# Kernel optimization log

Measured on AMD Instinct MI355X. Metric: run time of the kernel, lower is better.

The kernel has to match this reference:

```python
import jax, jax.numpy as jnp
import numpy as np

H = 512; VT = 10000; VN = 1000; ET = 256; EN = 256
A = 50; B = 8; L = 128; SOS = 0


def setup_inputs():
    key = jax.random.key(0)
    ks = jax.random.split(key, 12)
    g = lambda k, s: jax.random.normal(k, s, jnp.float32) * 0.02
    inp = {}
    inp["n_tensor"] = jax.random.randint(ks[0], (B, L), 0, VN)
    inp["t_tensor"] = jax.random.randint(ks[1], (B, L), 0, VT)
    inp["p_tensor"] = jax.random.randint(ks[2], (B, L), 0, L)
    # embedding tables; padding rows (padding_idx) zeroed as nn.Embedding init does
    inp["embN"] = g(ks[3], (VN, EN)).at[VN - 1].set(0.0)
    inp["embT"] = g(ks[4], (VT + A + 3, ET)).at[VT - 1].set(0.0)
    inp["W_hid"] = g(ks[5], (H, H)); inp["b_hid"] = jnp.zeros((H,), jnp.float32)
    inp["W_mem"] = g(ks[6], (H, H)); inp["b_mem"] = jnp.zeros((H,), jnp.float32)
    inp["v_w"] = g(ks[7], (H,)); inp["v_b"] = jnp.zeros((), jnp.float32)
    inp["W_ih"] = g(ks[8], (4 * H, EN + ET)); inp["W_hh"] = g(ks[9], (4 * H, H))
    inp["b_ih"] = jnp.zeros((4 * H,), jnp.float32); inp["b_hh"] = jnp.zeros((4 * H,), jnp.float32)
    inp["W_g"] = g(ks[10], (3 * H, VT + 3)); inp["b_g"] = jnp.zeros((VT + 3,), jnp.float32)
    inp["W_s"] = g(ks[11], (2 * H,)); inp["b_s"] = jnp.zeros((), jnp.float32)
    return inp


def _forward(embN, embT, W_hid, b_hid, W_mem, b_mem, v_w, v_b,
             W_ih, W_hh, b_ih, b_hh, W_g, b_g, W_s, b_s,
             n_tensor, t_tensor, p_tensor):
    full_mask = (n_tensor == VN - 1)                      # [B, L] eof mask
    sos = jnp.full((B, 1), SOS, n_tensor.dtype)
    n_in = jnp.concatenate([sos, n_tensor[:, :-1]], 1)    # teacher-forced inputs
    t_in = jnp.concatenate([sos, t_tensor[:, :-1]], 1)
    par = jnp.concatenate([jnp.zeros((B, 1), p_tensor.dtype), p_tensor[:, :-1]], 1)
    hs0 = jnp.zeros((B, L, H), jnp.float32)               # growing memory buffer
    h0 = jnp.zeros((B, H), jnp.float32)
    c0 = jnp.zeros((B, H), jnp.float32)
    barange = jnp.arange(B)
    arangeA = jnp.arange(A)

    def step(carry, xs):
        hs, h, c = carry
        t, n_t, t_t, p_t, tgt = xs
        # embedding gathers + single-layer LSTM cell (torch gate order i,f,g,o)
        x = jnp.concatenate([embN[n_t], embT[t_t]], 1)    # [B, EN+ET]
        gates = x @ W_ih.T + h @ W_hh.T + (b_ih + b_hh)
        i, f, gg, o = jnp.split(gates, 4, axis=1)
        c = jax.nn.sigmoid(f) * c + jax.nn.sigmoid(i) * jnp.tanh(gg)
        h = jax.nn.sigmoid(o) * jnp.tanh(c)
        # sliding-window memory hs[:, max(t-A,0):t], fixed-size slice + validity mask
        s = jnp.maximum(t - A, 0)
        mem = jax.lax.dynamic_slice(hs, (0, s, 0), (B, A, H))   # [B, A, H]
        fm = jax.lax.dynamic_slice(full_mask, (0, s), (B, A))   # [B, A]
        valid = (s + arangeA) < t                               # [A] positions already written
        mask = fm | ~valid[None, :]
        # additive attention: v^T tanh(W_hid h + W_mem mem)
        sc = jnp.tanh((h @ W_hid.T + b_hid)[:, None, :] + mem @ W_mem.T + b_mem)
        sc = sc @ v_w + v_b                                     # [B, A]
        sc = jnp.where(mask, -1e20, sc)
        attn = jax.nn.softmax(sc, axis=1)
        context = jnp.einsum('ba,bah->bh', attn, mem)
        h_parent = hs[barange, p_t]                             # per-batch gather on memory
        wt = jax.nn.log_softmax(jnp.concatenate([context, h, h_parent], 1) @ W_g + b_g, axis=1)
        log_attn = jax.nn.log_softmax(sc, axis=1)
        st = jax.nn.log_sigmoid(jnp.concatenate([context, h], 1) @ W_s + b_s)[:, None]  # [B,1]
        out = jnp.concatenate(
            [st + wt, jnp.log(jnp.clip(-jnp.expm1(st), 1e-18, 1e18)) + log_attn], 1)    # [B, VT+3+A]
        hs = hs.at[:, t].set(h)                                 # scatter new hidden into buffer
        loss_t = -jnp.take_along_axis(out, tgt[:, None], axis=1)[:, 0]  # NLLLoss(reduction='none')
        pred = jnp.argmax(out, axis=1)
        return (hs, h, c), (loss_t, pred)

    ts = jnp.arange(L)
    _, (losses, preds) = jax.lax.scan(
        step, (hs0, h0, c0), (ts, n_in.T, t_in.T, par.T, t_tensor.T))
    return losses.sum(), preds.T


def reference(n_tensor, t_tensor, p_tensor, embN, embT, W_hid, b_hid, W_mem, b_mem,
              v_w, v_b, W_ih, W_hh, b_ih, b_hh, W_g, b_g, W_s, b_s):
    return _forward(embN, embT, W_hid, b_hid, W_mem, b_mem, v_w, v_b,
                    W_ih, W_hh, b_ih, b_hh, W_g, b_g, W_s, b_s,
                    n_tensor, t_tensor, p_tensor)
```

## Files before the change

### kernel.cpp

```cpp
#include <hip/hip_runtime.h>
#include <hip/hip_bf16.h>
#include <math.h>

#define H_ 512
#define VN_ 1000
#define NG_ 10003
#define NGP_ 10240
#define NCHUNK 40
#define A_ 50
#define B_ 8
#define L_ 128
#define R_ 1024

typedef __hip_bfloat16 bf16;
typedef __attribute__((ext_vector_type(8))) short bf16x8;
typedef __attribute__((ext_vector_type(4))) float f32x4;

typedef union { unsigned long long u[2]; bf16x8 v; } frag_u;

__device__ __forceinline__ float fsig(float x) { return 1.0f / (1.0f + __expf(-x)); }
__device__ __forceinline__ float ftanh(float x) { return 1.0f - 2.0f / (1.0f + __expf(2.0f * x)); }

__device__ __forceinline__ short b16(float v) {
    __hip_bfloat16 h = __float2bfloat16(v);
    return *(short*)&h;
}

__device__ __forceinline__ unsigned long long ald(const unsigned long long* p) {
    return __hip_atomic_load(p, __ATOMIC_RELAXED, __HIP_MEMORY_SCOPE_AGENT);
}
__device__ __forceinline__ void ast32(unsigned int* p, unsigned int v) {
    __hip_atomic_store(p, v, __ATOMIC_RELAXED, __HIP_MEMORY_SCOPE_AGENT);
}

__global__ void k_init(int* flags, float* bkq,
                       const float* __restrict__ bmem, const float* __restrict__ bhid,
                       float* out)
{
    int i = blockIdx.x * 256 + threadIdx.x;
    if (i < 32)
        __hip_atomic_store(&flags[i], 0, __ATOMIC_RELAXED, __HIP_MEMORY_SCOPE_AGENT);
    if (i < 512) bkq[i] = bmem[i];
    else if (i < 1024) bkq[i] = bhid[i - 512];
    if (i == 0) out[0] = 0.f;
}

__global__ void k_w2b(const float* __restrict__ src, bf16* __restrict__ dst, int n)
{
    for (int i = blockIdx.x * blockDim.x + threadIdx.x; i < n; i += gridDim.x * blockDim.x)
        dst[i] = __float2bfloat16(src[i]);
}

__global__ void k_embed(const int* __restrict__ nt, const int* __restrict__ tt,
                        const float* __restrict__ embN, const float* __restrict__ embT,
                        bf16* __restrict__ X)
{
    int i = blockIdx.x * blockDim.x + threadIdx.x;
    int r = i >> 9, k = i & 511;
    int t = r >> 3, b = r & 7;
    float v;
    if (k < 256) {
        int id = (t == 0) ? 0 : nt[b * L_ + t - 1];
        v = embN[id * 256 + k];
    } else {
        int id = (t == 0) ? 0 : tt[b * L_ + t - 1];
        v = embT[id * 256 + (k - 256)];
    }
    X[i] = __float2bfloat16(v);
}

#define LSTM_BLOCKS 16
#define XTRA 240

#define DECLW(i) bf16x8 Wa##i, Wb##i;
#define LOADW(i) { \
    float4 a0 = *(const float4*)(wr0 + (i)*32); \
    float4 a1 = *(const float4*)(wr0 + (i)*32 + 4); \
    float4 c0 = *(const float4*)(wr1 + (i)*32); \
    float4 c1 = *(const float4*)(wr1 + (i)*32 + 4); \
    Wa##i[0]=b16(a0.x); Wa##i[1]=b16(a0.y); Wa##i[2]=b16(a0.z); Wa##i[3]=b16(a0.w); \
    Wa##i[4]=b16(a1.x); Wa##i[5]=b16(a1.y); Wa##i[6]=b16(a1.z); Wa##i[7]=b16(a1.w); \
    Wb##i[0]=b16(c0.x); Wb##i[1]=b16(c0.y); Wb##i[2]=b16(c0.z); Wb##i[3]=b16(c0.w); \
    Wb##i[4]=b16(c1.x); Wb##i[5]=b16(c1.y); Wb##i[6]=b16(c1.z); Wb##i[7]=b16(c1.w); }
#define LDF(i) frag_u fu##i; fu##i.u[0] = ald(src + (i)*128); fu##i.u[1] = ald(src + (i)*128 + 1);
#define MM(i) \
    acc0 = __builtin_amdgcn_mfma_f32_16x16x32_bf16(Wa##i, fu##i.v, acc0, 0, 0, 0); \
    acc1 = __builtin_amdgcn_mfma_f32_16x16x32_bf16(Wb##i, fu##i.v, acc1, 0, 0, 0);

__launch_bounds__(256, 1)
__global__ void k_lstm(const float* __restrict__ Whh, const float* __restrict__ xg,
                       bf16* __restrict__ hsb,
                       unsigned long long* __restrict__ bfr, int* __restrict__ flags,
                       const float* __restrict__ Wg, bf16* __restrict__ WT,
                       const float* __restrict__ Wmem, const float* __restrict__ Whid,
                       bf16* __restrict__ wkq)
{
    __shared__ float gl[4][32][9];
    __shared__ short S[64][65];
    const int tid  = threadIdx.x;
    const int x    = blockIdx.x;

    if (x >= LSTM_BLOCKS) {
        for (int i = (x - LSTM_BLOCKS) * 256 + tid; i < 2 * 512 * 512; i += XTRA * 256) {
            float v = (i < 512 * 512) ? Wmem[i] : Whid[i - 512 * 512];
            wkq[i] = __float2bfloat16(v);
        }
        const int c = tid & 63;
        const int r0 = (tid >> 6) * 16;
        const int n_l = tid >> 2;
        const int kq = (tid & 3) * 16;
        for (int tile = x - LSTM_BLOCKS; tile < 160 * 24; tile += XTRA) {
            int n0 = (tile % 160) * 64, k0 = (tile / 160) * 64;
            __syncthreads();
            #pragma unroll
            for (int i = 0; i < 16; ++i) {
                int k = r0 + i;
                int n = n0 + c;
                float v = (n < NG_) ? Wg[(size_t)(k0 + k) * NG_ + n] : 0.f;
                S[c][k] = b16(v);
            }
            __syncthreads();
            bf16* dst = WT + (size_t)(n0 + n_l) * 1536 + k0 + kq;
            #pragma unroll
            for (int j = 0; j < 2; ++j) {
                bf16x8 v;
                #pragma unroll
                for (int e = 0; e < 8; ++e) v[e] = S[n_l][kq + j * 8 + e];
                *(bf16x8*)(dst + j * 8) = v;
            }
        }
        return;
    }

    const int lane = tid & 63;
    const int w    = tid >> 6;
    const int m_l  = lane & 15;
    const int kg   = lane >> 4;
    const int n    = lane & 15;
    unsigned int* bfr32 = (unsigned int*)bfr;

    const float* wr0 = Whh + (size_t)(w * 512 + x * 32 + m_l) * 512 + kg * 8;
    const float* wr1 = wr0 + (size_t)16 * 512;
    DECLW(0)  DECLW(1)  DECLW(2)  DECLW(3)  DECLW(4)  DECLW(5)  DECLW(6)  DECLW(7)
    DECLW(8)  DECLW(9)  DECLW(10) DECLW(11) DECLW(12) DECLW(13) DECLW(14) DECLW(15)
    LOADW(0)  LOADW(1)  LOADW(2)  LOADW(3)  LOADW(4)  LOADW(5)  LOADW(6)  LOADW(7)
    LOADW(8)  LOADW(9)  LOADW(10) LOADW(11) LOADW(12) LOADW(13) LOADW(14) LOADW(15)
    asm volatile("" : "+v"(Wa0), "+v"(Wb0), "+v"(Wa1), "+v"(Wb1), "+v"(Wa2), "+v"(Wb2),
                      "+v"(Wa3), "+v"(Wb3), "+v"(Wa4), "+v"(Wb4), "+v"(Wa5), "+v"(Wb5),
                      "+v"(Wa6), "+v"(Wb6), "+v"(Wa7), "+v"(Wb7));
    asm volatile("" : "+v"(Wa8), "+v"(Wb8), "+v"(Wa9), "+v"(Wb9), "+v"(Wa10), "+v"(Wb10),
                      "+v"(Wa11), "+v"(Wb11), "+v"(Wa12), "+v"(Wb12), "+v"(Wa13), "+v"(Wb13),
                      "+v"(Wa14), "+v"(Wb14), "+v"(Wa15), "+v"(Wb15));

    const int u_l = tid >> 3;
    const int b   = tid & 7;
    float creg = 0.f;
    int fearly = 0;

    for (int t = 0; t < L_; ++t) {
        const float* xr = xg + ((size_t)t * B_ + b) * 2048 + x * 32 + u_l;
        float xi = xr[0], xf = xr[512], xgg = xr[1024], xo = xr[1536];

        f32x4 acc0 = {0.f, 0.f, 0.f, 0.f};
        f32x4 acc1 = {0.f, 0.f, 0.f, 0.f};
        if (t > 0) {
            if (!__all(fearly >= t)) {
                for (;;) {
                    int v = (lane < LSTM_BLOCKS)
                        ? __hip_atomic_load(&flags[lane], __ATOMIC_RELAXED, __HIP_MEMORY_SCOPE_AGENT)
                        : t;
                    if (__all(v >= t)) break;
                    __builtin_amdgcn_s_sleep(1);
                }
            }
            const unsigned long long* src =
                bfr + (size_t)((t + 1) & 1) * 2048 + lane * 2;
            LDF(0)  LDF(1)  LDF(2)  LDF(3)  LDF(4)  LDF(5)  LDF(6)  LDF(7)
            LDF(8)  LDF(9)  LDF(10) LDF(11) LDF(12) LDF(13) LDF(14) LDF(15)
            __builtin_amdgcn_sched_barrier(0);
            MM(0)  MM(1)  MM(2)  MM(3)  MM(4)  MM(5)  MM(6)  MM(7)
            MM(8)  MM(9)  MM(10) MM(11) MM(12) MM(13) MM(14) MM(15)
        }
        if (n < 8) {
            #pragma unroll
            for (int i = 0; i < 4; ++i) {
                gl[w][kg * 4 + i][n]      = acc0[i];
                gl[w][16 + kg * 4 + i][n] = acc1[i];
            }
        }
        __syncthreads();
        float gi = gl[0][u_l][b] + xi;
        float gf = gl[1][u_l][b] + xf;
        float gg = gl[2][u_l][b] + xgg;
        float go = gl[3][u_l][b] + xo;
        float iv = fsig(gi), fv = fsig(gf), gv = ftanh(gg), ov = fsig(go);
        creg = fv * creg + iv * gv;
        float h = ov * ftanh(creg);
        float h2 = __shfl_xor(h, 8);
        unsigned pay = 0;
        if ((u_l & 1) == 0) {
            pay = (unsigned)(unsigned short)b16(h)
                | ((unsigned)(unsigned short)b16(h2) << 16);
            int q = u_l >> 3, p = (u_l & 7) >> 1;
            ast32(bfr32 + (size_t)(t & 1) * 4096 + x * 256 + (b + 16 * q) * 4 + p, pay);
        }
        fearly = (lane < LSTM_BLOCKS && lane != x)
            ? __hip_atomic_load(&flags[lane], __ATOMIC_RELAXED, __HIP_MEMORY_SCOPE_AGENT)
            : 0x7FFFFFFF;
        asm volatile("s_waitcnt vmcnt(0)" ::: "memory");
        __syncthreads();
        if (tid == 0)
            __hip_atomic_store(&flags[x], t + 1, __ATOMIC_RELAXED, __HIP_MEMORY_SCOPE_AGENT);
        if ((u_l & 1) == 0)
            *(unsigned int*)(hsb + (size_t)(t * B_ + b) * 512 + x * 32 + u_l) = pay;
    }
}

__launch_bounds__(256)
__global__ void k_attn(const bf16* __restrict__ hsb, const float* __restrict__ kmq,
                       const float* __restrict__ vw,
                       const float* __restrict__ vb, const int* __restrict__ nt,
                       const int* __restrict__ pt, const float* __restrict__ Wsv,
                       const float* __restrict__ bs, bf16* __restrict__ gcat,
                       float* __restrict__ logattn, float* __restrict__ stbuf)
{
    const int r = blockIdx.x;
    const int t = r >> 3, b = r & 7;
    const int tid = threadIdx.x;
    const int lane = tid & 63, wave = tid >> 6;
    int s = t - A_; if (s < 0) s = 0;
    __shared__ float qv[512];
    __shared__ float vwl[512];
    __shared__ float sc[A_];
    __shared__ float attn[A_];
    __shared__ float red[4];
    for (int i = tid; i < 512; i += 256) {
        qv[i] = kmq[(size_t)r * 1024 + 512 + i];
        vwl[i] = vw[i];
    }
    __syncthreads();
    for (int a = wave; a < A_; a += 4) {
        int pos = s + a;
        float v = -1e20f;
        bool masked = (pos >= t) || (nt[b * L_ + pos] == VN_ - 1);
        if (!masked) {
            const float* kr = kmq + (size_t)(pos * B_ + b) * 1024;
            float p = 0.f;
            for (int k = lane; k < 512; k += 64)
                p += vwl[k] * ftanh(qv[k] + kr[k]);
            for (int off = 32; off; off >>= 1) p += __shfl_down(p, off);
            v = p + vb[0];
        }
        if (lane == 0) sc[a] = v;
    }
    __syncthreads();
    if (tid < 64) {
        float v = (tid < A_) ? sc[tid] : -INFINITY;
        float m = v;
        for (int off = 32; off; off >>= 1) m = fmaxf(m, __shfl_xor(m, off));
        float e = (tid < A_) ? expf(v - m) : 0.f;
        float d = e;
        for (int off = 32; off; off >>= 1) d += __shfl_xor(d, off);
        if (tid < A_) {
            attn[tid] = e / d;
            logattn[(size_t)r * A_ + tid] = (v - m) - logf(d);
        }
    }
    __syncthreads();
    const int k0 = tid * 2;
    float c0 = 0.f, c1 = 0.f;
    for (int a = 0; a < A_; ++a) {
        int pos = s + a;
        if (pos >= t) break;
        float w = attn[a];
        unsigned u = *(const unsigned*)((const unsigned short*)hsb + (size_t)(pos * B_ + b) * 512 + k0);
        c0 += w * __uint_as_float(u << 16);
        c1 += w * __uint_as_float(u & 0xffff0000u);
    }
    unsigned ucur = *(const unsigned*)((const unsigned short*)hsb + (size_t)(t * B_ + b) * 512 + k0);
    int par = (t == 0) ? 0 : pt[b * L_ + t - 1];
    unsigned upar = 0;
    if (par < t)
        upar = *(const unsigned*)((const unsigned short*)hsb + (size_t)(par * B_ + b) * 512 + k0);
    float hx = __uint_as_float(ucur << 16), hy = __uint_as_float(ucur & 0xffff0000u);
    bf16* g = gcat + (size_t)r * 1536;
    g[k0]     = __float2bfloat16(c0);
    g[k0 + 1] = __float2bfloat16(c1);
    *(unsigned*)(g + 512 + k0)  = ucur;
    *(unsigned*)(g + 1024 + k0) = upar;
    float part = c0 * Wsv[k0] + c1 * Wsv[k0 + 1]
               + hx * Wsv[512 + k0] + hy * Wsv[512 + k0 + 1];
    for (int off = 32; off; off >>= 1) part += __shfl_down(part, off);
    if (lane == 0) red[wave] = part;
    __syncthreads();
    if (tid == 0) {
        float z = red[0] + red[1] + red[2] + red[3] + bs[0];
        stbuf[r] = -log1pf(expf(-z));
    }
}

__launch_bounds__(256, 2)
__global__ void k_gemm128b(const bf16* __restrict__ Ag, const bf16* __restrict__ Bg,
                           const float* __restrict__ b1, const float* __restrict__ b2,
                           float* __restrict__ C, int N, int K)
{
    __shared__ short As[128 * 32];
    __shared__ short Bs[128 * 32];
    const int tid = threadIdx.x;
    const int lane = tid & 63, wave = tid >> 6;
    const int wr = wave >> 1, wc = wave & 1;
    const int m0 = blockIdx.y * 128, n0 = blockIdx.x * 128;
    f32x4 acc[4][4] = {};
    for (int k0 = 0; k0 < K; k0 += 32) {
        __syncthreads();
        #pragma unroll
        for (int h = 0; h < 2; ++h) {
            int o = tid + h * 256;
            int row = o >> 2;
            int kc = (o & 3) ^ (row & 3);
            const bf16* ga = Ag + (size_t)(m0 + row) * K + k0 + kc * 8;
            const bf16* gb = Bg + (size_t)(n0 + row) * K + k0 + kc * 8;
            unsigned ldso = h * 4096 + wave * 1024;
            __builtin_amdgcn_global_load_lds(
                (const __attribute__((address_space(1))) void*)ga,
                (__attribute__((address_space(3))) void*)((char*)As + ldso), 16, 0, 0);
            __builtin_amdgcn_global_load_lds(
                (const __attribute__((address_space(1))) void*)gb,
                (__attribute__((address_space(3))) void*)((char*)Bs + ldso), 16, 0, 0);
        }
        asm volatile("s_waitcnt vmcnt(0)" ::: "memory");
        __syncthreads();
        bf16x8 af[4], bf[4];
        #pragma unroll
        for (int mi = 0; mi < 4; ++mi) {
            int ra = wr * 64 + mi * 16 + (lane & 15);
            af[mi] = *(const bf16x8*)&As[ra * 32 + (((lane >> 4) ^ (ra & 3)) * 8)];
        }
        #pragma unroll
        for (int ni = 0; ni < 4; ++ni) {
            int rb = wc * 64 + ni * 16 + (lane & 15);
            bf[ni] = *(const bf16x8*)&Bs[rb * 32 + (((lane >> 4) ^ (rb & 3)) * 8)];
        }
        #pragma unroll
        for (int mi = 0; mi < 4; ++mi)
            #pragma unroll
            for (int ni = 0; ni < 4; ++ni)
                acc[mi][ni] = __builtin_amdgcn_mfma_f32_16x16x32_bf16(af[mi], bf[ni], acc[mi][ni], 0, 0, 0);
    }
    const int col = lane & 15, rq = (lane >> 4) * 4;
    #pragma unroll
    for (int mi = 0; mi < 4; ++mi)
        #pragma unroll
        for (int ni = 0; ni < 4; ++ni) {
            int nn = n0 + wc * 64 + ni * 16 + col;
            float bias = (b1 ? b1[nn] : 0.f) + (b2 ? b2[nn] : 0.f);
            #pragma unroll
            for (int i = 0; i < 4; ++i)
                C[(size_t)(m0 + wr * 64 + mi * 16 + rq + i) * N + nn] = acc[mi][ni][i] + bias;
        }
}

__launch_bounds__(256, 2)
__global__ void k_gemm128p(const bf16* __restrict__ Ag, const bf16* __restrict__ Bg,
                           const float* __restrict__ bg, const int* __restrict__ tt,
                           float* __restrict__ pst)
{
    __shared__ short As[128 * 32];
    __shared__ short Bs[128 * 32];
    __shared__ float bgl[256];
    __shared__ float mrg[128][6];
    const int tid = threadIdx.x;
    const int lane = tid & 63, wave = tid >> 6;
    const int wr = wave >> 1, wc = wave & 1;
    const int col16 = lane & 15, rq = (lane >> 4) * 4;
    const int chunk = blockIdx.x;
    const int m0 = blockIdx.y * 128;
    const int K = 1536;

    bgl[tid] = (chunk * 256 + tid < NG_) ? bg[chunk * 256 + tid] : -INFINITY;

    float M[4][4], S[4][4], AV[4][4], TGT[4][4]; int AI[4][4]; int tgt[4][4];
    #pragma unroll
    for (int mi = 0; mi < 4; ++mi)
        #pragma unroll
        for (int i = 0; i < 4; ++i) {
            M[mi][i] = -INFINITY; S[mi][i] = 0.f; AV[mi][i] = -INFINITY;
            TGT[mi][i] = -INFINITY; AI[mi][i] = 0x7FFFFFFF;
            int row = m0 + wr * 64 + mi * 16 + rq + i;
            tgt[mi][i] = tt[(row & 7) * L_ + (row >> 3)];
        }

    for (int nt = 0; nt < 2; ++nt) {
        const int n0 = chunk * 256 + nt * 128;
        f32x4 acc[4][4] = {};
        for (int k0 = 0; k0 < K; k0 += 32) {
            __syncthreads();
            #pragma unroll
            for (int h = 0; h < 2; ++h) {
                int o = tid + h * 256;
                int row = o >> 2;
                int kc = (o & 3) ^ (row & 3);
                const bf16* ga = Ag + (size_t)(m0 + row) * K + k0 + kc * 8;
                const bf16* gb = Bg + (size_t)(n0 + row) * K + k0 + kc * 8;
                unsigned ldso = h * 4096 + wave * 1024;
                __builtin_amdgcn_global_load_lds(
                    (const __attribute__((address_space(1))) void*)ga,
                    (__attribute__((address_space(3))) void*)((char*)As + ldso), 16, 0, 0);
                __builtin_amdgcn_global_load_lds(
                    (const __attribute__((address_space(1))) void*)gb,
                    (__attribute__((address_space(3))) void*)((char*)Bs + ldso), 16, 0, 0);
            }
            asm volatile("s_waitcnt vmcnt(0)" ::: "memory");
            __syncthreads();
            bf16x8 af[4], bf[4];
            #pragma unroll
            for (int mi = 0; mi < 4; ++mi) {
                int ra = wr * 64 + mi * 16 + col16;
                af[mi] = *(const bf16x8*)&As[ra * 32 + (((lane >> 4) ^ (ra & 3)) * 8)];
            }
            #pragma unroll
            for (int ni = 0; ni < 4; ++ni) {
                int rb = wc * 64 + ni * 16 + col16;
                bf[ni] = *(const bf16x8*)&Bs[rb * 32 + (((lane >> 4) ^ (rb & 3)) * 8)];
            }
            #pragma unroll
            for (int mi = 0; mi < 4; ++mi)
                #pragma unroll
                for (int ni = 0; ni < 4; ++ni)
                    acc[mi][ni] = __builtin_amdgcn_mfma_f32_16x16x32_bf16(af[mi], bf[ni], acc[mi][ni], 0, 0, 0);
        }
        #pragma unroll
        for (int mi = 0; mi < 4; ++mi)
            #pragma unroll
            for (int i = 0; i < 4; ++i) {
                float v[4]; int nn[4];
                #pragma unroll
                for (int ni = 0; ni < 4; ++ni) {
                    int cl = nt * 128 + wc * 64 + ni * 16 + col16;
                    v[ni] = acc[mi][ni][i] + bgl[cl];
                    nn[ni] = chunk * 256 + cl;
                }
                float lv = v[0]; int li = nn[0];
                #pragma unroll
                for (int ni = 1; ni < 4; ++ni)
                    if (v[ni] > lv) { lv = v[ni]; li = nn[ni]; }
                #pragma unroll
                for (int off = 1; off < 16; off <<= 1) {
                    float ov = __shfl_xor(lv, off); int oi = __shfl_xor(li, off);
                    if (ov > lv || (ov == lv && oi < li)) { lv = ov; li = oi; }
                }
                float nM = fmaxf(M[mi][i], lv);
                float add = 0.f;
                if (nM != -INFINITY) {
                    #pragma unroll
                    for (int ni = 0; ni < 4; ++ni) add += expf(v[ni] - nM);
                    #pragma unroll
                    for (int off = 1; off < 16; off <<= 1) add += __shfl_xor(add, off);
                }
                S[mi][i] = ((S[mi][i] > 0.f) ? S[mi][i] * expf(M[mi][i] - nM) : 0.f) + add;
                M[mi][i] = nM;
                if (lv > AV[mi][i] || (lv == AV[mi][i] && li < AI[mi][i])) {
                    AV[mi][i] = lv; AI[mi][i] = li;
                }
                float tv = -INFINITY;
                #pragma unroll
                for (int ni = 0; ni < 4; ++ni)
                    if (nn[ni] == tgt[mi][i]) tv = v[ni];
                #pragma unroll
                for (int off = 1; off < 16; off <<= 1)
                    tv = fmaxf(tv, __shfl_xor(tv, off));
                TGT[mi][i] = fmaxf(TGT[mi][i], tv);
            }
    }
    __syncthreads();
    if (wc == 1 && col16 == 0) {
        #pragma unroll
        for (int mi = 0; mi < 4; ++mi)
            #pragma unroll
            for (int i = 0; i < 4; ++i) {
                int rl = wr * 64 + mi * 16 + rq + i;
                mrg[rl][0] = M[mi][i]; mrg[rl][1] = S[mi][i];
                mrg[rl][2] = AV[mi][i]; mrg[rl][3] = __int_as_float(AI[mi][i]);
                mrg[rl][4] = TGT[mi][i];
            }
    }
    __syncthreads();
    if (wc == 0 && col16 == 0) {
        #pragma unroll
        for (int mi = 0; mi < 4; ++mi)
            #pragma unroll
            for (int i = 0; i < 4; ++i) {
                int rl = wr * 64 + mi * 16 + rq + i;
                float oM = mrg[rl][0], oS = mrg[rl][1], oAV = mrg[rl][2];
                int oAI = __float_as_int(mrg[rl][3]);
                float oT = mrg[rl][4];
                float nM = fmaxf(M[mi][i], oM);
                float s1 = (S[mi][i] > 0.f) ? S[mi][i] * expf(M[mi][i] - nM) : 0.f;
                float s2 = (oS > 0.f) ? oS * expf(oM - nM) : 0.f;
                float av = AV[mi][i]; int ai = AI[mi][i];
                if (oAV > av || (oAV == av && oAI < ai)) { av = oAV; ai = oAI; }
                float* p = pst + ((size_t)chunk * R_ + (m0 + rl)) * 8;
                p[0] = nM; p[1] = s1 + s2; p[2] = av;
                p[3] = __int_as_float(ai); p[4] = fmaxf(TGT[mi][i], oT);
            }
    }
}

__launch_bounds__(64)
__global__ void k_loss2(const float* __restrict__ pst, const float* __restrict__ logattn,
                        const float* __restrict__ stbuf, float* __restrict__ out)
{
    const int r = blockIdx.x;
    const int lane = threadIdx.x;
    float M = -INFINITY, S = 0.f, AV = -INFINITY, TGT = -INFINITY;
    int AI = 0x7FFFFFFF;
    if (lane < NCHUNK) {
        const float* p = pst + ((size_t)lane * R_ + r) * 8;
        M = p[0]; S = p[1]; AV = p[2]; AI = __float_as_int(p[3]); TGT = p[4];
    }
    for (int off = 32; off; off >>= 1) {
        float oM = __shfl_xor(M, off), oS = __shfl_xor(S, off);
        float oAV = __shfl_xor(AV, off), oT = __shfl_xor(TGT, off);
        int oAI = __shfl_xor(AI, off);
        float nM = fmaxf(M, oM);
        float s1 = (S > 0.f) ? S * expf(M - nM) : 0.f;
        float s2 = (oS > 0.f) ? oS * expf(oM - nM) : 0.f;
        M = nM; S = s1 + s2;
        if (oAV > AV || (oAV == AV && oAI < AI)) { AV = oAV; AI = oAI; }
        TGT = fmaxf(TGT, oT);
    }
    if (lane == 0) {
        float lse = M + logf(S);
        float st = stbuf[r];
        const float* la = logattn + (size_t)r * A_;
        float lamax = la[0]; int aidx = 0;
        for (int a = 1; a < A_; ++a) if (la[a] > lamax) { lamax = la[a]; aidx = a; }
        float e1 = -expm1f(st);
        e1 = fminf(fmaxf(e1, 1e-18f), 1e18f);
        float lm = logf(e1);
        float p1 = st + M - lse;
        float p2 = lm + lamax;
        int pred = (p1 >= p2) ? AI : (NG_ + aidx);
        float loss = -(st + TGT - lse);
        atomicAdd(&out[0], loss);
        int t = r >> 3, b = r & 7;
        out[1 + b * L_ + t] = (float)pred;
    }
}

extern "C" void kernel_launch(void* const* d_in, const int* in_sizes, int n_in,
                              void* d_out, int out_size, void* d_ws, size_t ws_size,
                              hipStream_t stream)
{
    (void)in_sizes; (void)n_in; (void)out_size; (void)ws_size;
    const int*   nt    = (const int*)d_in[0];
    const int*   tt    = (const int*)d_in[1];
    const int*   pt    = (const int*)d_in[2];
    const float* embN  = (const float*)d_in[3];
    const float* embT  = (const float*)d_in[4];
    const float* W_hid = (const float*)d_in[5];
    const float* b_hid = (const float*)d_in[6];
    const float* W_mem = (const float*)d_in[7];
    const float* b_mem = (const float*)d_in[8];
    const float* v_w   = (const float*)d_in[9];
    const float* v_b   = (const float*)d_in[10];
    const float* W_ih  = (const float*)d_in[11];
    const float* W_hh  = (const float*)d_in[12];
    const float* b_ih  = (const float*)d_in[13];
    const float* b_hh  = (const float*)d_in[14];
    const float* W_g   = (const float*)d_in[15];
    const float* b_g   = (const float*)d_in[16];
    const float* W_s   = (const float*)d_in[17];
    const float* b_s   = (const float*)d_in[18];
    float* out = (float*)d_out;

    char* ws = (char*)d_ws;
    size_t o = 0;
    bf16*  WGT  = (bf16*)(ws + o);  o += (size_t)NGP_ * 1536 * 2;
    float* XG   = (float*)(ws + o); o += (size_t)R_ * 2048 * 4;
    bf16*  HSB  = (bf16*)(ws + o);  o += (size_t)R_ * H_ * 2;
    float* KMQ  = (float*)(ws + o); o += (size_t)R_ * 1024 * 4;
    bf16*  WKQ  = (bf16*)(ws + o);  o += (size_t)1024 * 512 * 2;
    float* BKQ  = (float*)(ws + o); o += (size_t)1024 * 4;
    bf16*  XB   = (bf16*)(ws + o);  o += (size_t)R_ * H_ * 2;
    bf16*  WIHB = (bf16*)(ws + o);  o += (size_t)2048 * 512 * 2;
    bf16*  GC   = (bf16*)(ws + o);  o += (size_t)R_ * 1536 * 2;
    float* LA   = (float*)(ws + o); o += (size_t)R_ * A_ * 4;
    float* ST   = (float*)(ws + o); o += (size_t)R_ * 4;
    float* PST  = (float*)(ws + o); o += (size_t)NCHUNK * R_ * 8 * 4;
    unsigned long long* BFR = (unsigned long long*)(ws + o); o += (size_t)4096 * 8;
    int*   FLG  = (int*)(ws + o);   o += 256;

    k_init<<<4, 256, 0, stream>>>(FLG, BKQ, b_mem, b_hid, out);
    k_w2b<<<1024, 256, 0, stream>>>(W_ih, WIHB, 2048 * 512);
    k_embed<<<R_ * H_ / 256, 256, 0, stream>>>(nt, tt, embN, embT, XB);
    k_gemm128b<<<dim3(2048 / 128, R_ / 128), 256, 0, stream>>>(XB, WIHB, b_ih, b_hh, XG, 2048, 512);
    k_lstm<<<LSTM_BLOCKS + XTRA, 256, 0, stream>>>(W_hh, XG, HSB, BFR, FLG,
                                                   W_g, WGT, W_mem, W_hid, WKQ);
    k_gemm128b<<<dim3(1024 / 128, R_ / 128), 256, 0, stream>>>(HSB, WKQ, BKQ, nullptr, KMQ, 1024, 512);
    k_attn<<<R_, 256, 0, stream>>>(HSB, KMQ, v_w, v_b, nt, pt, W_s, b_s, GC, LA, ST);
    k_gemm128p<<<dim3(NCHUNK, R_ / 128), 256, 0, stream>>>(GC, WGT, b_g, tt, PST);
    k_loss2<<<R_, 64, 0, stream>>>(PST, LA, ST, out);
}
```

Baseline: 603.8 us.

## Fuse key/query projection and attention into persistent LSTM mega-kernel as per-step consumers

Merges the LSTM recurrence, the memory/hidden projection GEMM and the attention kernel into one persistent launch. 128 consumer blocks, one per timestep, wait on flags set by the LSTM blocks. Each then computes its own key/query projection with scalar FMAs and runs attention for all batches, overlapping that work with the serial recurrence. Per-wave flags replace per-block flags. The risks are scalar GEMM throughput, spin-wait contention, and deadlock if not all 256 blocks are co-resident.

```diff
diff --git a/kernel.cpp b/kernel.cpp
--- a/kernel.cpp
+++ b/kernel.cpp
@@ -25,21 +25,42 @@
     __hip_bfloat16 h = __float2bfloat16(v);
     return *(short*)&h;
 }
+__device__ __forceinline__ float bf2f(unsigned short u) {
+    return __uint_as_float(((unsigned)u) << 16);
+}
 
 __device__ __forceinline__ unsigned long long ald(const unsigned long long* p) {
     return __hip_atomic_load(p, __ATOMIC_RELAXED, __HIP_MEMORY_SCOPE_AGENT);
 }
+__device__ __forceinline__ unsigned ald32(const unsigned* p) {
+    return __hip_atomic_load(p, __ATOMIC_RELAXED, __HIP_MEMORY_SCOPE_AGENT);
+}
+__device__ __forceinline__ int aldi(const int* p) {
+    return __hip_atomic_load(p, __ATOMIC_RELAXED, __HIP_MEMORY_SCOPE_AGENT);
+}
+__device__ __forceinline__ float aldf(const float* p) {
+    return __hip_atomic_load(p, __ATOMIC_RELAXED, __HIP_MEMORY_SCOPE_AGENT);
+}
 __device__ __forceinline__ void ast32(unsigned int* p, unsigned int v) {
     __hip_atomic_store(p, v, __ATOMIC_RELAXED, __HIP_MEMORY_SCOPE_AGENT);
 }
-
-__global__ void k_init(int* flags, float* bkq,
+__device__ __forceinline__ void asti(int* p, int v) {
+    __hip_atomic_store(p, v, __ATOMIC_RELAXED, __HIP_MEMORY_SCOPE_AGENT);
+}
+__device__ __forceinline__ void astf(float* p, float v) {
+    __hip_atomic_store(p, v, __ATOMIC_RELAXED, __HIP_MEMORY_SCOPE_AGENT);
+}
+
+#define KMFLG 64
+#define WKQFLG 192
+
+__global__ void k_init(int* flg, float* bkq,
                        const float* __restrict__ bmem, const float* __restrict__ bhid,
                        float* out)
 {
     int i = blockIdx.x * 256 + threadIdx.x;
-    if (i < 32)
-        __hip_atomic_store(&flags[i], 0, __ATOMIC_RELAXED, __HIP_MEMORY_SCOPE_AGENT);
+    if (i < 256)
+        __hip_atomic_store(&flg[i], 0, __ATOMIC_RELAXED, __HIP_MEMORY_SCOPE_AGENT);
     if (i < 512) bkq[i] = bmem[i];
     else if (i < 1024) bkq[i] = bhid[i - 512];
     if (i == 0) out[0] = 0.f;
@@ -70,7 +91,8 @@
 }
 
 #define LSTM_BLOCKS 16
-#define XTRA 240
+#define CONS 128
+#define TRB 112
 
 #define DECLW(i) bf16x8 Wa##i, Wb##i;
 #define LOADW(i) { \
@@ -88,28 +110,133 @@
     acc1 = __builtin_amdgcn_mfma_f32_16x16x32_bf16(Wb##i, fu##i.v, acc1, 0, 0, 0);
 
 __launch_bounds__(256, 1)
-__global__ void k_lstm(const float* __restrict__ Whh, const float* __restrict__ xg,
+__global__ void k_mega(const float* __restrict__ Whh, const float* __restrict__ xg,
                        bf16* __restrict__ hsb,
-                       unsigned long long* __restrict__ bfr, int* __restrict__ flags,
+                       unsigned long long* __restrict__ bfr, int* __restrict__ flg,
                        const float* __restrict__ Wg, bf16* __restrict__ WT,
                        const float* __restrict__ Wmem, const float* __restrict__ Whid,
-                       bf16* __restrict__ wkq)
+                       bf16* __restrict__ wkq, float* __restrict__ kmf,
+                       const int* __restrict__ nt, const int* __restrict__ pt,
+                       const float* __restrict__ vw, const float* __restrict__ vb,
+                       const float* __restrict__ Wsv, const float* __restrict__ bs,
+                       const float* __restrict__ bkq,
+                       bf16* __restrict__ gcat, float* __restrict__ logattn,
+                       float* __restrict__ stbuf)
 {
     __shared__ float gl[4][32][9];
     __shared__ short S[64][65];
+    __shared__ float hq[512][8];
+    __shared__ float qb[512][9];
+    __shared__ float vwl[512];
+    __shared__ float sc[8][52];
+    __shared__ float attnw[8][52];
+    __shared__ float red[4];
+
     const int tid  = threadIdx.x;
     const int x    = blockIdx.x;
-
-    if (x >= LSTM_BLOCKS) {
-        for (int i = (x - LSTM_BLOCKS) * 256 + tid; i < 2 * 512 * 512; i += XTRA * 256) {
-            float v = (i < 512 * 512) ? Wmem[i] : Whid[i - 512 * 512];
-            wkq[i] = __float2bfloat16(v);
-        }
+    const int lane = tid & 63;
+    const int wave = tid >> 6;
+
+    if (x < LSTM_BLOCKS) {
+        const int w    = wave;
+        const int m_l  = lane & 15;
+        const int kg   = lane >> 4;
+        const int n    = lane & 15;
+        unsigned int* bfr32 = (unsigned int*)bfr;
+        unsigned int* hsb32 = (unsigned int*)hsb;
+
+        const float* wr0 = Whh + (size_t)(w * 512 + x * 32 + m_l) * 512 + kg * 8;
+        const float* wr1 = wr0 + (size_t)16 * 512;
+        DECLW(0)  DECLW(1)  DECLW(2)  DECLW(3)  DECLW(4)  DECLW(5)  DECLW(6)  DECLW(7)
+        DECLW(8)  DECLW(9)  DECLW(10) DECLW(11) DECLW(12) DECLW(13) DECLW(14) DECLW(15)
+        LOADW(0)  LOADW(1)  LOADW(2)  LOADW(3)  LOADW(4)  LOADW(5)  LOADW(6)  LOADW(7)
+        LOADW(8)  LOADW(9)  LOADW(10) LOADW(11) LOADW(12) LOADW(13) LOADW(14) LOADW(15)
+        asm volatile("" : "+v"(Wa0), "+v"(Wb0), "+v"(Wa1), "+v"(Wb1), "+v"(Wa2), "+v"(Wb2),
+                          "+v"(Wa3), "+v"(Wb3), "+v"(Wa4), "+v"(Wb4), "+v"(Wa5), "+v"(Wb5),
+                          "+v"(Wa6), "+v"(Wb6), "+v"(Wa7), "+v"(Wb7));
+        asm volatile("" : "+v"(Wa8), "+v"(Wb8), "+v"(Wa9), "+v"(Wb9), "+v"(Wa10), "+v"(Wb10),
+                          "+v"(Wa11), "+v"(Wb11), "+v"(Wa12), "+v"(Wb12), "+v"(Wa13), "+v"(Wb13),
+                          "+v"(Wa14), "+v"(Wb14), "+v"(Wa15), "+v"(Wb15));
+
+        const int u_l = tid >> 3;
+        const int b   = tid & 7;
+        float creg = 0.f;
+        int fearly = 0;
+
+        for (int t = 0; t < L_; ++t) {
+            const float* xr = xg + ((size_t)t * B_ + b) * 2048 + x * 32 + u_l;
+            float xi = xr[0], xf = xr[512], xgg = xr[1024], xo = xr[1536];
+
+            f32x4 acc0 = {0.f, 0.f, 0.f, 0.f};
+            f32x4 acc1 = {0.f, 0.f, 0.f, 0.f};
+            if (t > 0) {
+                if (!__all(fearly >= t)) {
+                    for (;;) {
+                        int v = aldi(&flg[lane]);
+                        if (__all(v >= t)) break;
+                        __builtin_amdgcn_s_sleep(1);
+                    }
+                }
+                const unsigned long long* src =
+                    bfr + (size_t)((t + 1) & 1) * 2048 + lane * 2;
+                LDF(0)  LDF(1)  LDF(2)  LDF(3)  LDF(4)  LDF(5)  LDF(6)  LDF(7)
+                LDF(8)  LDF(9)  LDF(10) LDF(11) LDF(12) LDF(13) LDF(14) LDF(15)
+                __builtin_amdgcn_sched_barrier(0);
+                MM(0)  MM(1)  MM(2)  MM(3)  MM(4)  MM(5)  MM(6)  MM(7)
+                MM(8)  MM(9)  MM(10) MM(11) MM(12) MM(13) MM(14) MM(15)
+            }
+            if (n < 8) {
+                #pragma unroll
+                for (int i = 0; i < 4; ++i) {
+                    gl[w][kg * 4 + i][n]      = acc0[i];
+                    gl[w][16 + kg * 4 + i][n] = acc1[i];
+                }
+            }
+            __syncthreads();
+            float gi = gl[0][u_l][b] + xi;
+            float gf = gl[1][u_l][b] + xf;
+            float gg = gl[2][u_l][b] + xgg;
+            float go = gl[3][u_l][b] + xo;
+            float iv = fsig(gi), fv = fsig(gf), gv = ftanh(gg), ov = fsig(go);
+            creg = fv * creg + iv * gv;
+            float h = ov * ftanh(creg);
+            float h2 = __shfl_xor(h, 8);
+            if ((u_l & 1) == 0) {
+                unsigned pay = (unsigned)(unsigned short)b16(h)
+                             | ((unsigned)(unsigned short)b16(h2) << 16);
+                int q = u_l >> 3, p = (u_l & 7) >> 1;
+                ast32(bfr32 + (size_t)(t & 1) * 4096 + x * 256 + (b + 16 * q) * 4 + p, pay);
+                ast32(hsb32 + (size_t)(t * B_ + b) * 256 + (x * 32 + u_l) / 2, pay);
+            }
+            fearly = (lane != x * 4 + w) ? aldi(&flg[lane]) : 0x7FFFFFFF;
+            asm volatile("s_waitcnt vmcnt(0)" ::: "memory");
+            if (lane == 0)
+                asti(&flg[x * 4 + w], t + 1);
+        }
+        return;
+    }
+
+    if (x >= LSTM_BLOCKS + CONS) {
+        const int d = x - LSTM_BLOCKS - CONS;
+        unsigned* wk32 = (unsigned*)wkq;
+        for (int i = d * 256 + tid; i < 262144; i += TRB * 256) {
+            int e = i * 2;
+            float v0 = (e < 262144) ? Wmem[e] : Whid[e - 262144];
+            float v1 = (e + 1 < 262144) ? Wmem[e + 1] : Whid[e + 1 - 262144];
+            unsigned u = (unsigned)(unsigned short)b16(v0)
+                       | ((unsigned)(unsigned short)b16(v1) << 16);
+            ast32(wk32 + i, u);
+        }
+        asm volatile("s_waitcnt vmcnt(0)" ::: "memory");
+        __syncthreads();
+        if (tid == 0)
+            __hip_atomic_fetch_add(&flg[WKQFLG], 1, __ATOMIC_RELAXED, __HIP_MEMORY_SCOPE_AGENT);
+
         const int c = tid & 63;
         const int r0 = (tid >> 6) * 16;
         const int n_l = tid >> 2;
         const int kq = (tid & 3) * 16;
-        for (int tile = x - LSTM_BLOCKS; tile < 160 * 24; tile += XTRA) {
+        for (int tile = d; tile < 160 * 24; tile += TRB) {
             int n0 = (tile % 160) * 64, k0 = (tile / 160) * 64;
             __syncthreads();
             #pragma unroll
@@ -132,170 +259,145 @@
         return;
     }
 
-    const int lane = tid & 63;
-    const int w    = tid >> 6;
-    const int m_l  = lane & 15;
-    const int kg   = lane >> 4;
-    const int n    = lane & 15;
-    unsigned int* bfr32 = (unsigned int*)bfr;
-
-    const float* wr0 = Whh + (size_t)(w * 512 + x * 32 + m_l) * 512 + kg * 8;
-    const float* wr1 = wr0 + (size_t)16 * 512;
-    DECLW(0)  DECLW(1)  DECLW(2)  DECLW(3)  DECLW(4)  DECLW(5)  DECLW(6)  DECLW(7)
-    DECLW(8)  DECLW(9)  DECLW(10) DECLW(11) DECLW(12) DECLW(13) DECLW(14) DECLW(15)
-    LOADW(0)  LOADW(1)  LOADW(2)  LOADW(3)  LOADW(4)  LOADW(5)  LOADW(6)  LOADW(7)
-    LOADW(8)  LOADW(9)  LOADW(10) LOADW(11) LOADW(12) LOADW(13) LOADW(14) LOADW(15)
-    asm volatile("" : "+v"(Wa0), "+v"(Wb0), "+v"(Wa1), "+v"(Wb1), "+v"(Wa2), "+v"(Wb2),
-                      "+v"(Wa3), "+v"(Wb3), "+v"(Wa4), "+v"(Wb4), "+v"(Wa5), "+v"(Wb5),
-                      "+v"(Wa6), "+v"(Wb6), "+v"(Wa7), "+v"(Wb7));
-    asm volatile("" : "+v"(Wa8), "+v"(Wb8), "+v"(Wa9), "+v"(Wb9), "+v"(Wa10), "+v"(Wb10),
-                      "+v"(Wa11), "+v"(Wb11), "+v"(Wa12), "+v"(Wb12), "+v"(Wa13), "+v"(Wb13),
-                      "+v"(Wa14), "+v"(Wb14), "+v"(Wa15), "+v"(Wb15));
-
-    const int u_l = tid >> 3;
-    const int b   = tid & 7;
-    float creg = 0.f;
-    int fearly = 0;
-
-    for (int t = 0; t < L_; ++t) {
-        const float* xr = xg + ((size_t)t * B_ + b) * 2048 + x * 32 + u_l;
-        float xi = xr[0], xf = xr[512], xgg = xr[1024], xo = xr[1536];
-
-        f32x4 acc0 = {0.f, 0.f, 0.f, 0.f};
-        f32x4 acc1 = {0.f, 0.f, 0.f, 0.f};
-        if (t > 0) {
-            if (!__all(fearly >= t)) {
-                for (;;) {
-                    int v = (lane < LSTM_BLOCKS)
-                        ? __hip_atomic_load(&flags[lane], __ATOMIC_RELAXED, __HIP_MEMORY_SCOPE_AGENT)
-                        : t;
-                    if (__all(v >= t)) break;
-                    __builtin_amdgcn_s_sleep(1);
+    {
+        const int t = x - LSTM_BLOCKS;
+        int s = t - A_; if (s < 0) s = 0;
+        const int cnt = t - s;
+        const unsigned* hsb32 = (const unsigned*)hsb;
+
+        if (wave == 0) {
+            for (;;) {
+                int v = aldi(&flg[lane]);
+                if (__all(v >= t + 1)) break;
+                __builtin_amdgcn_s_sleep(32);
+            }
+        }
+        __syncthreads();
+        for (int i = tid; i < 2048; i += 256) {
+            int b = i >> 8, p = i & 255;
+            unsigned u = ald32(hsb32 + (size_t)(t * B_ + b) * 256 + p);
+            hq[p * 2][b]     = __uint_as_float(u << 16);
+            hq[p * 2 + 1][b] = __uint_as_float(u & 0xffff0000u);
+        }
+        if (tid == 0) {
+            while (aldi(&flg[WKQFLG]) < TRB) __builtin_amdgcn_s_sleep(16);
+        }
+        __syncthreads();
+        {
+            const int j0 = tid * 4;
+            float av[4][8];
+            #pragma unroll
+            for (int c = 0; c < 4; ++c)
+                #pragma unroll
+                for (int b = 0; b < 8; ++b) av[c][b] = 0.f;
+            const bf16x8* wr0p = (const bf16x8*)(wkq + (size_t)(j0 + 0) * 512);
+            const bf16x8* wr1p = (const bf16x8*)(wkq + (size_t)(j0 + 1) * 512);
+            const bf16x8* wr2p = (const bf16x8*)(wkq + (size_t)(j0 + 2) * 512);
+            const bf16x8* wr3p = (const bf16x8*)(wkq + (size_t)(j0 + 3) * 512);
+            for (int kc = 0; kc < 64; ++kc) {
+                bf16x8 w0 = wr0p[kc], w1 = wr1p[kc], w2 = wr2p[kc], w3 = wr3p[kc];
+                #pragma unroll
+                for (int e = 0; e < 8; ++e) {
+                    int k = kc * 8 + e;
+                    float f0 = bf2f((unsigned short)w0[e]);
+                    float f1 = bf2f((unsigned short)w1[e]);
+                    float f2 = bf2f((unsigned short)w2[e]);
+                    float f3 = bf2f((unsigned short)w3[e]);
+                    #pragma unroll
+                    for (int b = 0; b < 8; ++b) {
+                        float hb = hq[k][b];
+                        av[0][b] += f0 * hb; av[1][b] += f1 * hb;
+                        av[2][b] += f2 * hb; av[3][b] += f3 * hb;
+                    }
                 }
             }
-            const unsigned long long* src =
-                bfr + (size_t)((t + 1) & 1) * 2048 + lane * 2;
-            LDF(0)  LDF(1)  LDF(2)  LDF(3)  LDF(4)  LDF(5)  LDF(6)  LDF(7)
-            LDF(8)  LDF(9)  LDF(10) LDF(11) LDF(12) LDF(13) LDF(14) LDF(15)
-            __builtin_amdgcn_sched_barrier(0);
-            MM(0)  MM(1)  MM(2)  MM(3)  MM(4)  MM(5)  MM(6)  MM(7)
-            MM(8)  MM(9)  MM(10) MM(11) MM(12) MM(13) MM(14) MM(15)
-        }
-        if (n < 8) {
-            #pragma unroll
-            for (int i = 0; i < 4; ++i) {
-                gl[w][kg * 4 + i][n]      = acc0[i];
-                gl[w][16 + kg * 4 + i][n] = acc1[i];
-            }
-        }
-        __syncthreads();
-        float gi = gl[0][u_l][b] + xi;
-        float gf = gl[1][u_l][b] + xf;
-        float gg = gl[2][u_l][b] + xgg;
-        float go = gl[3][u_l][b] + xo;
-        float iv = fsig(gi), fv = fsig(gf), gv = ftanh(gg), ov = fsig(go);
-        creg = fv * creg + iv * gv;
-        float h = ov * ftanh(creg);
-        float h2 = __shfl_xor(h, 8);
-        unsigned pay = 0;
-        if ((u_l & 1) == 0) {
-            pay = (unsigned)(unsigned short)b16(h)
-                | ((unsigned)(unsigned short)b16(h2) << 16);
-            int q = u_l >> 3, p = (u_l & 7) >> 1;
-            ast32(bfr32 + (size_t)(t & 1) * 4096 + x * 256 + (b + 16 * q) * 4 + p, pay);
-        }
-        fearly = (lane < LSTM_BLOCKS && lane != x)
-            ? __hip_atomic_load(&flags[lane], __ATOMIC_RELAXED, __HIP_MEMORY_SCOPE_AGENT)
-            : 0x7FFFFFFF;
+            #pragma unroll
+            for (int c = 0; c < 4; ++c) {
+                int j = j0 + c;
+                float bj = bkq[j];
+                if (j < 512) {
+                    #pragma unroll
+                    for (int b = 0; b < 8; ++b)
+                        astf(kmf + ((size_t)t * B_ + b) * 512 + j, av[c][b] + bj);
+                } else {
+                    #pragma unroll
+                    for (int b = 0; b < 8; ++b)
+                        qb[j - 512][b] = av[c][b] + bj;
+                }
+            }
+        }
         asm volatile("s_waitcnt vmcnt(0)" ::: "memory");
         __syncthreads();
-        if (tid == 0)
-            __hip_atomic_store(&flags[x], t + 1, __ATOMIC_RELAXED, __HIP_MEMORY_SCOPE_AGENT);
-        if ((u_l & 1) == 0)
-            *(unsigned int*)(hsb + (size_t)(t * B_ + b) * 512 + x * 32 + u_l) = pay;
-    }
-}
-
-__launch_bounds__(256)
-__global__ void k_attn(const bf16* __restrict__ hsb, const float* __restrict__ kmq,
-                       const float* __restrict__ vw,
-                       const float* __restrict__ vb, const int* __restrict__ nt,
-                       const int* __restrict__ pt, const float* __restrict__ Wsv,
-                       const float* __restrict__ bs, bf16* __restrict__ gcat,
-                       float* __restrict__ logattn, float* __restrict__ stbuf)
-{
-    const int r = blockIdx.x;
-    const int t = r >> 3, b = r & 7;
-    const int tid = threadIdx.x;
-    const int lane = tid & 63, wave = tid >> 6;
-    int s = t - A_; if (s < 0) s = 0;
-    __shared__ float qv[512];
-    __shared__ float vwl[512];
-    __shared__ float sc[A_];
-    __shared__ float attn[A_];
-    __shared__ float red[4];
-    for (int i = tid; i < 512; i += 256) {
-        qv[i] = kmq[(size_t)r * 1024 + 512 + i];
-        vwl[i] = vw[i];
-    }
-    __syncthreads();
-    for (int a = wave; a < A_; a += 4) {
-        int pos = s + a;
-        float v = -1e20f;
-        bool masked = (pos >= t) || (nt[b * L_ + pos] == VN_ - 1);
-        if (!masked) {
-            const float* kr = kmq + (size_t)(pos * B_ + b) * 1024;
-            float p = 0.f;
-            for (int k = lane; k < 512; k += 64)
-                p += vwl[k] * ftanh(qv[k] + kr[k]);
-            for (int off = 32; off; off >>= 1) p += __shfl_down(p, off);
-            v = p + vb[0];
-        }
-        if (lane == 0) sc[a] = v;
-    }
-    __syncthreads();
-    if (tid < 64) {
-        float v = (tid < A_) ? sc[tid] : -INFINITY;
-        float m = v;
-        for (int off = 32; off; off >>= 1) m = fmaxf(m, __shfl_xor(m, off));
-        float e = (tid < A_) ? expf(v - m) : 0.f;
-        float d = e;
-        for (int off = 32; off; off >>= 1) d += __shfl_xor(d, off);
-        if (tid < A_) {
-            attn[tid] = e / d;
-            logattn[(size_t)r * A_ + tid] = (v - m) - logf(d);
-        }
-    }
-    __syncthreads();
-    const int k0 = tid * 2;
-    float c0 = 0.f, c1 = 0.f;
-    for (int a = 0; a < A_; ++a) {
-        int pos = s + a;
-        if (pos >= t) break;
-        float w = attn[a];
-        unsigned u = *(const unsigned*)((const unsigned short*)hsb + (size_t)(pos * B_ + b) * 512 + k0);
-        c0 += w * __uint_as_float(u << 16);
-        c1 += w * __uint_as_float(u & 0xffff0000u);
-    }
-    unsigned ucur = *(const unsigned*)((const unsigned short*)hsb + (size_t)(t * B_ + b) * 512 + k0);
-    int par = (t == 0) ? 0 : pt[b * L_ + t - 1];
-    unsigned upar = 0;
-    if (par < t)
-        upar = *(const unsigned*)((const unsigned short*)hsb + (size_t)(par * B_ + b) * 512 + k0);
-    float hx = __uint_as_float(ucur << 16), hy = __uint_as_float(ucur & 0xffff0000u);
-    bf16* g = gcat + (size_t)r * 1536;
-    g[k0]     = __float2bfloat16(c0);
-    g[k0 + 1] = __float2bfloat16(c1);
-    *(unsigned*)(g + 512 + k0)  = ucur;
-    *(unsigned*)(g + 1024 + k0) = upar;
-    float part = c0 * Wsv[k0] + c1 * Wsv[k0 + 1]
-               + hx * Wsv[512 + k0] + hy * Wsv[512 + k0 + 1];
-    for (int off = 32; off; off >>= 1) part += __shfl_down(part, off);
-    if (lane == 0) red[wave] = part;
-    __syncthreads();
-    if (tid == 0) {
-        float z = red[0] + red[1] + red[2] + red[3] + bs[0];
-        stbuf[r] = -log1pf(expf(-z));
+        if (tid == 0) asti(&flg[KMFLG + t], 1);
+        if (wave == 0 && cnt > 0) {
+            for (;;) {
+                int v = (lane < cnt) ? aldi(&flg[KMFLG + s + lane]) : 1;
+                if (__all(v >= 1)) break;
+                __builtin_amdgcn_s_sleep(16);
+            }
+        }
+        for (int i = tid; i < 512; i += 256) vwl[i] = vw[i];
+        __syncthreads();
+        const float vb0 = vb[0];
+        for (int idx = wave; idx < 400; idx += 4) {
+            int a = idx >> 3, b = idx & 7, pos = s + a;
+            float v = -1e20f;
+            if (pos < t && nt[b * L_ + pos] != VN_ - 1) {
+                const float* kr = kmf + ((size_t)pos * B_ + b) * 512;
+                float p = 0.f;
+                for (int k = lane; k < 512; k += 64)
+                    p += vwl[k] * ftanh(qb[k][b] + aldf(kr + k));
+                for (int off = 32; off; off >>= 1) p += __shfl_down(p, off);
+                v = p + vb0;
+            }
+            if (lane == 0) sc[b][a] = v;
+        }
+        __syncthreads();
+        for (int b = wave; b < 8; b += 4) {
+            float v = (lane < A_) ? sc[b][lane] : -INFINITY;
+            float m = v;
+            for (int off = 32; off; off >>= 1) m = fmaxf(m, __shfl_xor(m, off));
+            float e = (lane < A_) ? expf(v - m) : 0.f;
+            float d = e;
+            for (int off = 32; off; off >>= 1) d += __shfl_xor(d, off);
+            if (lane < A_) {
+                attnw[b][lane] = e / d;
+                logattn[(size_t)(t * B_ + b) * A_ + lane] = (v - m) - logf(d);
+            }
+        }
+        __syncthreads();
+        const int k0 = tid * 2;
+        for (int b = 0; b < 8; ++b) {
+            float c0 = 0.f, c1 = 0.f;
+            for (int a = 0; a < A_; ++a) {
+                int pos = s + a;
+                if (pos >= t) break;
+                float w = attnw[b][a];
+                unsigned u = ald32(hsb32 + (size_t)(pos * B_ + b) * 256 + tid);
+                c0 += w * __uint_as_float(u << 16);
+                c1 += w * __uint_as_float(u & 0xffff0000u);
+            }
+            unsigned ucur = ald32(hsb32 + (size_t)(t * B_ + b) * 256 + tid);
+            int par = (t == 0) ? 0 : pt[b * L_ + t - 1];
+            unsigned upar = 0;
+            if (par < t) upar = ald32(hsb32 + (size_t)(par * B_ + b) * 256 + tid);
+            float hx = __uint_as_float(ucur << 16), hy = __uint_as_float(ucur & 0xffff0000u);
+            bf16* g = gcat + (size_t)(t * B_ + b) * 1536;
+            g[k0]     = __float2bfloat16(c0);
+            g[k0 + 1] = __float2bfloat16(c1);
+            *(unsigned*)(g + 512 + k0)  = ucur;
+            *(unsigned*)(g + 1024 + k0) = upar;
+            float part = c0 * Wsv[k0] + c1 * Wsv[k0 + 1]
+                       + hx * Wsv[512 + k0] + hy * Wsv[512 + k0 + 1];
+            for (int off = 32; off; off >>= 1) part += __shfl_down(part, off);
+            if (lane == 0) red[wave] = part;
+            __syncthreads();
+            if (tid == 0) {
+                float z = red[0] + red[1] + red[2] + red[3] + bs[0];
+                stbuf[t * B_ + b] = -log1pf(expf(-z));
+            }
+            __syncthreads();
+        }
     }
 }
 
@@ -579,7 +681,7 @@
     bf16*  WGT  = (bf16*)(ws + o);  o += (size_t)NGP_ * 1536 * 2;
     float* XG   = (float*)(ws + o); o += (size_t)R_ * 2048 * 4;
     bf16*  HSB  = (bf16*)(ws + o);  o += (size_t)R_ * H_ * 2;
-    float* KMQ  = (float*)(ws + o); o += (size_t)R_ * 1024 * 4;
+    float* KMF  = (float*)(ws + o); o += (size_t)R_ * H_ * 4;
     bf16*  WKQ  = (bf16*)(ws + o);  o += (size_t)1024 * 512 * 2;
     float* BKQ  = (float*)(ws + o); o += (size_t)1024 * 4;
     bf16*  XB   = (bf16*)(ws + o);  o += (size_t)R_ * H_ * 2;
@@ -589,16 +691,15 @@
     float* ST   = (float*)(ws + o); o += (size_t)R_ * 4;
     float* PST  = (float*)(ws + o); o += (size_t)NCHUNK * R_ * 8 * 4;
     unsigned long long* BFR = (unsigned long long*)(ws + o); o += (size_t)4096 * 8;
-    int*   FLG  = (int*)(ws + o);   o += 256;
+    int*   FLG  = (int*)(ws + o);   o += 1024;
 
     k_init<<<4, 256, 0, stream>>>(FLG, BKQ, b_mem, b_hid, out);
     k_w2b<<<1024, 256, 0, stream>>>(W_ih, WIHB, 2048 * 512);
     k_embed<<<R_ * H_ / 256, 256, 0, stream>>>(nt, tt, embN, embT, XB);
     k_gemm128b<<<dim3(2048 / 128, R_ / 128), 256, 0, stream>>>(XB, WIHB, b_ih, b_hh, XG, 2048, 512);
-    k_lstm<<<LSTM_BLOCKS + XTRA, 256, 0, stream>>>(W_hh, XG, HSB, BFR, FLG,
-                                                   W_g, WGT, W_mem, W_hid, WKQ);
-    k_gemm128b<<<dim3(1024 / 128, R_ / 128), 256, 0, stream>>>(HSB, WKQ, BKQ, nullptr, KMQ, 1024, 512);
-    k_attn<<<R_, 256, 0, stream>>>(HSB, KMQ, v_w, v_b, nt, pt, W_s, b_s, GC, LA, ST);
+    k_mega<<<LSTM_BLOCKS + CONS + TRB, 256, 0, stream>>>(
+        W_hh, XG, HSB, BFR, FLG, W_g, WGT, W_mem, W_hid, WKQ, KMF,
+        nt, pt, v_w, v_b, W_s, b_s, BKQ, GC, LA, ST);
     k_gemm128p<<<dim3(NCHUNK, R_ / 128), 256, 0, stream>>>(GC, WGT, b_g, tt, PST);
     k_loss2<<<R_, 64, 0, stream>>>(PST, LA, ST, out);
 }
```

After: 944.9 us. 1.57x slower.
